# Kernel optimization log

Hardware: AMD Instinct MI355X
Metric: run time of the kernel (lower is better)

The kernel has to match this reference:

```python
import jax, jax.numpy as jnp
import numpy as np
from jax import lax

B, T, D, LSTM, N_MELS, SPK, NOISE = 256, 600, 256, 512, 80, 256, 64
MAX_R = 10
FC1 = 256
FC2 = D // 2  # 128
FILTERS, KSIZE = 32, 31


def _lin(k, out_d, in_d):
    return jax.random.normal(k, (out_d, in_d), jnp.float32) * 0.02


def setup_inputs() -> dict:
    key = jax.random.key(0)
    ks = list(jax.random.split(key, 40))
    nk = iter(ks)
    inp = {
        "encoder_seq": jax.random.normal(next(nk), (B, T, D), jnp.float32),
        "encoder_seq_proj": jax.random.normal(next(nk), (B, T, D), jnp.float32),
        "prenet_in": jax.random.normal(next(nk), (B, N_MELS), jnp.float32),
        "attn_hidden": jax.random.normal(next(nk), (B, D), jnp.float32),
        "rnn1_hidden": jax.random.normal(next(nk), (B, LSTM), jnp.float32),
        "rnn2_hidden": jax.random.normal(next(nk), (B, LSTM), jnp.float32),
        "rnn1_cell": jax.random.normal(next(nk), (B, LSTM), jnp.float32),
        "rnn2_cell": jax.random.normal(next(nk), (B, LSTM), jnp.float32),
        "context_vec": jax.random.normal(next(nk), (B, D), jnp.float32),
        "speaker_embedding": jax.random.normal(next(nk), (B, SPK), jnp.float32),
        "noise_embedding": jax.random.normal(next(nk), (B, NOISE), jnp.float32),
        "attn_cumulative": jax.random.uniform(next(nk), (B, T), jnp.float32),
        "attn_prev": jax.random.uniform(next(nk), (B, T), jnp.float32),
        "phone_len": jax.random.randint(next(nk), (B,), 1, T + 1),
        # PreNet
        "fc1_w": _lin(next(nk), FC1, N_MELS + NOISE), "fc1_b": jnp.zeros((FC1,), jnp.float32),
        "fc2_w": _lin(next(nk), FC2, FC1), "fc2_b": jnp.zeros((FC2,), jnp.float32),
        # LSA
        "conv_w": jax.random.normal(next(nk), (FILTERS, 2, KSIZE), jnp.float32) * 0.1,
        "L_w": _lin(next(nk), D, FILTERS), "L_b": jnp.zeros((D,), jnp.float32),
        "W_w": _lin(next(nk), D, D), "W_b": jnp.zeros((D,), jnp.float32),
        "v_w": _lin(next(nk), 1, D),
        # attn GRU: input = D + D//2 + SPK
        "gru_wih": _lin(next(nk), 3 * D, D + FC2 + SPK), "gru_whh": _lin(next(nk), 3 * D, D),
        "gru_bih": jnp.zeros((3 * D,), jnp.float32), "gru_bhh": jnp.zeros((3 * D,), jnp.float32),
        # rnn_input Linear: 2*D + SPK + NOISE -> LSTM
        "rnn_in_w": _lin(next(nk), LSTM, 2 * D + SPK + NOISE), "rnn_in_b": jnp.zeros((LSTM,), jnp.float32),
        # two LSTMCells
        "l1_wih": _lin(next(nk), 4 * LSTM, LSTM), "l1_whh": _lin(next(nk), 4 * LSTM, LSTM),
        "l1_bih": jnp.zeros((4 * LSTM,), jnp.float32), "l1_bhh": jnp.zeros((4 * LSTM,), jnp.float32),
        "l2_wih": _lin(next(nk), 4 * LSTM, LSTM), "l2_whh": _lin(next(nk), 4 * LSTM, LSTM),
        "l2_bih": jnp.zeros((4 * LSTM,), jnp.float32), "l2_bhh": jnp.zeros((4 * LSTM,), jnp.float32),
        # mel projection (no bias)
        "mel_w": _lin(next(nk), N_MELS * MAX_R, LSTM),
        "r": 2,
    }
    return inp


def _gru(x, h, wih, whh, bih, bhh):
    gi = x @ wih.T + bih
    gh = h @ whh.T + bhh
    i_r, i_z, i_n = jnp.split(gi, 3, axis=-1)
    h_r, h_z, h_n = jnp.split(gh, 3, axis=-1)
    r = jax.nn.sigmoid(i_r + h_r)
    z = jax.nn.sigmoid(i_z + h_z)
    n = jnp.tanh(i_n + r * h_n)
    return (1.0 - z) * n + z * h


def _lstm(x, h, c, wih, whh, bih, bhh):
    g = x @ wih.T + bih + h @ whh.T + bhh
    i, f, gg, o = jnp.split(g, 4, axis=-1)
    c_new = jax.nn.sigmoid(f) * c + jax.nn.sigmoid(i) * jnp.tanh(gg)
    h_new = jax.nn.sigmoid(o) * jnp.tanh(c_new)
    return h_new, c_new


def reference(encoder_seq, encoder_seq_proj, prenet_in, attn_hidden, rnn1_hidden,
              rnn2_hidden, rnn1_cell, rnn2_cell, context_vec, speaker_embedding,
              noise_embedding, attn_cumulative, attn_prev, phone_len,
              fc1_w, fc1_b, fc2_w, fc2_b, conv_w, L_w, L_b, W_w, W_b, v_w,
              gru_wih, gru_whh, gru_bih, gru_bhh, rnn_in_w, rnn_in_b,
              l1_wih, l1_whh, l1_bih, l1_bhh, l2_wih, l2_whh, l2_bih, l2_bhh,
              mel_w, r):
    # PreNet (eval-mode: dropout omitted for a deterministic reference)
    p = jnp.concatenate([prenet_in, noise_embedding], axis=-1)
    p = jax.nn.relu(p @ fc1_w.T + fc1_b)
    prenet_out = jax.nn.relu(p @ fc2_w.T + fc2_b)

    # attention GRU
    attn_rnn_in = jnp.concatenate([context_vec, prenet_out, speaker_embedding], axis=-1)
    attn_hidden = _gru(attn_rnn_in, attn_hidden, gru_wih, gru_whh, gru_bih, gru_bhh)

    # location-sensitive attention (t > 0 step; state passed explicitly)
    pq = (attn_hidden @ W_w.T + W_b)[:, None, :]                     # [B,1,D]
    location = jnp.stack([attn_cumulative, attn_prev], axis=1)       # [B,2,T]
    loc = lax.conv_general_dilated(location, conv_w, (1,), [((KSIZE - 1) // 2,) * 2],
                                   dimension_numbers=("NCH", "OIH", "NCH"))  # [B,F,T]
    pl = jnp.einsum("bft,df->btd", loc, L_w) + L_b                   # [B,T,D]
    u = jnp.einsum("btd,od->bt", jnp.tanh(pq + encoder_seq_proj + pl), v_w)
    mask = jnp.arange(T)[None, :] < phone_len[:, None]
    u = jnp.where(mask, u, -1e9)
    scores_bt = jax.nn.softmax(u, axis=1)                            # [B,T]
    scores = scores_bt[:, None, :]                                   # [B,1,T]

    context_vec = jnp.einsum("bt,btd->bd", scores_bt, encoder_seq)   # [B,D]

    x = jnp.concatenate([context_vec, attn_hidden, speaker_embedding, noise_embedding], axis=1)
    x = x @ rnn_in_w.T + rnn_in_b

    rnn1_hidden, rnn1_cell = _lstm(x, rnn1_hidden, rnn1_cell, l1_wih, l1_whh, l1_bih, l1_bhh)
    x = x + rnn1_hidden
    rnn2_hidden, rnn2_cell = _lstm(x, rnn2_hidden, rnn2_cell, l2_wih, l2_whh, l2_bih, l2_bhh)
    x = x + rnn2_hidden

    mels = (x @ mel_w.T).reshape(B, N_MELS, MAX_R)[:, :, :r]
    return (mels, scores, attn_hidden, rnn1_hidden, rnn2_hidden, rnn1_cell, rnn2_cell, context_vec)
```

## Files before the change

kernel.cpp:

```cpp
#include <hip/hip_runtime.h>
#include <hip/hip_bf16.h>
#include <cstdint>

#define B_ 256
#define T_ 600
#define D_ 256

typedef __attribute__((ext_vector_type(8))) short bf16x8;
typedef __attribute__((ext_vector_type(4))) float f32x4;

__device__ __forceinline__ float fast_sigmoid(float x) {
    return __fdividef(1.0f, 1.0f + __expf(-x));
}
__device__ __forceinline__ float fast_tanh(float x) {
    return 1.0f - __fdividef(2.0f, __expf(2.0f * x) + 1.0f);
}
__device__ __forceinline__ ushort f2bf(float f) {
    unsigned u = __float_as_uint(f);
    u += 0x7FFF + ((u >> 16) & 1);
    return (ushort)(u >> 16);
}

__global__ __launch_bounds__(256) void prenet_kernel(
    const float* __restrict__ pre_in, const float* __restrict__ noise,
    const float* __restrict__ w1, const float* __restrict__ b1,
    const float* __restrict__ w2, const float* __restrict__ b2,
    const float* __restrict__ ctx_in, const float* __restrict__ spk,
    const float* __restrict__ L_w, ushort* __restrict__ Lw16,
    float* __restrict__ Xgru, float* __restrict__ Xrnn)
{
    __shared__ float xin[144];
    __shared__ float p1[256];
    int b = blockIdx.x, t = threadIdx.x;
    if (b == 0) {
        for (int o = t; o < 8192; o += 256) {
            int dt = o >> 9;
            int ln = (o >> 3) & 63;
            int j  = o & 7;
            int in_idx = (dt * 16 + (ln & 15)) * 32 + (ln >> 4) * 8 + j;
            Lw16[o] = f2bf(L_w[in_idx]);
        }
    }
    float s = spk[b * 256 + t];
    Xgru[b * 640 + t] = ctx_in[b * 256 + t];
    Xgru[b * 640 + 384 + t] = s;
    Xrnn[b * 832 + 512 + t] = s;
    if (t < 64) Xrnn[b * 832 + 768 + t] = noise[b * 64 + t];
    if (t < 80) xin[t] = pre_in[b * 80 + t];
    else if (t < 144) xin[t] = noise[b * 64 + (t - 80)];
    __syncthreads();
    float acc = b1[t];
    const float4* w = (const float4*)(w1 + t * 144);
    const float4* xi = (const float4*)xin;
#pragma unroll 9
    for (int k = 0; k < 36; ++k) {
        float4 wv = w[k]; float4 xv = xi[k];
        acc += wv.x * xv.x + wv.y * xv.y + wv.z * xv.z + wv.w * xv.w;
    }
    p1[t] = fmaxf(acc, 0.f);
    __syncthreads();
    if (t < 128) {
        float a2 = b2[t];
        const float4* w2v = (const float4*)(w2 + t * 256);
        const float4* pv = (const float4*)p1;
#pragma unroll 8
        for (int k = 0; k < 64; ++k) {
            float4 wv = w2v[k]; float4 xv = pv[k];
            a2 += wv.x * xv.x + wv.y * xv.y + wv.z * xv.z + wv.w * xv.w;
        }
        Xgru[b * 640 + 256 + t] = fmaxf(a2, 0.f);
    }
}

__global__ __launch_bounds__(256) void convert_w(
    const float* __restrict__ w1ih, const float* __restrict__ w1hh,
    const float* __restrict__ w2ih, const float* __restrict__ w2hh,
    ushort* __restrict__ wcat1, ushort* __restrict__ wcat2)
{
    int n = blockIdx.x & 2047;
    int layer = blockIdx.x >> 11;
    int t = threadIdx.x;
    const float* wih = layer ? w2ih : w1ih;
    const float* whh = layer ? w2hh : w1hh;
    ushort* dst = layer ? wcat2 : wcat1;
    const float* src = (t < 128) ? (wih + (size_t)n * 512 + t * 4)
                                 : (whh + (size_t)n * 512 + (t - 128) * 4);
    float4 v = *(const float4*)src;
    ushort4 o;
    o.x = f2bf(v.x); o.y = f2bf(v.y); o.z = f2bf(v.z); o.w = f2bf(v.w);
    *(ushort4*)&dst[(size_t)n * 1024 + t * 4] = o;
}

__global__ __launch_bounds__(256) void cast_xh(
    const float* __restrict__ x, const float* __restrict__ h,
    ushort* __restrict__ xh)
{
    int b = blockIdx.x, t = threadIdx.x;
    float2 xv = *(const float2*)&x[b * 512 + t * 2];
    float2 hv = *(const float2*)&h[b * 512 + t * 2];
    xh[(size_t)b * 1024 + t * 2 + 0] = f2bf(xv.x);
    xh[(size_t)b * 1024 + t * 2 + 1] = f2bf(xv.y);
    xh[(size_t)b * 1024 + 512 + t * 2 + 0] = f2bf(hv.x);
    xh[(size_t)b * 1024 + 512 + t * 2 + 1] = f2bf(hv.y);
}

__global__ __launch_bounds__(256) void mfma_gemm(
    const ushort* __restrict__ A16, const ushort* __restrict__ B16,
    float* __restrict__ G0, float* __restrict__ G1)
{
    int tid = threadIdx.x;
    int lane = tid & 63, wv = tid >> 6;
    int m0 = blockIdx.x * 32;
    int n0 = blockIdx.y * 64;
    int kbase = blockIdx.z * 512;
    float* Gout = blockIdx.z ? G1 : G0;
    int wm = wv >> 1, wn = wv & 1;
    int cl = lane & 15, ko = (lane >> 4) * 8;

    const ushort* ap  = A16 + (size_t)(m0 + wm * 16 + cl) * 1024 + kbase + ko;
    const ushort* bp0 = B16 + (size_t)(n0 + wn * 32 + cl) * 1024 + kbase + ko;
    const ushort* bp1 = bp0 + (size_t)16 * 1024;

    f32x4 acc0 = {0.f, 0.f, 0.f, 0.f};
    f32x4 acc1 = {0.f, 0.f, 0.f, 0.f};
#pragma unroll
    for (int ks = 0; ks < 16; ++ks) {
        bf16x8 a  = *(const bf16x8*)(ap  + ks * 32);
        bf16x8 b0 = *(const bf16x8*)(bp0 + ks * 32);
        bf16x8 b1 = *(const bf16x8*)(bp1 + ks * 32);
        acc0 = __builtin_amdgcn_mfma_f32_16x16x32_bf16(a, b0, acc0, 0, 0, 0);
        acc1 = __builtin_amdgcn_mfma_f32_16x16x32_bf16(a, b1, acc1, 0, 0, 0);
    }
    int orow = m0 + wm * 16 + (lane >> 4) * 4;
    int ocol = n0 + wn * 32 + cl;
#pragma unroll
    for (int r2 = 0; r2 < 4; ++r2) {
        Gout[(size_t)(orow + r2) * 2048 + ocol]      = acc0[r2];
        Gout[(size_t)(orow + r2) * 2048 + ocol + 16] = acc1[r2];
    }
}

__global__ __launch_bounds__(256) void gemm16(
    const float* __restrict__ A1, int K1, const float* __restrict__ B1,
    const float* __restrict__ A2, int K2, const float* __restrict__ B2,
    const float* __restrict__ bias, float* __restrict__ C, int N)
{
    __shared__ float As[16][17];
    __shared__ float Bs[16][68];
    int tid = threadIdx.x;
    int m0 = blockIdx.x * 16, n0 = blockIdx.y * 64;
    int tm = tid >> 4, tn = tid & 15;
    int lr = tid >> 2, lq = tid & 3;
    int ar = tid >> 2;
    float acc[4] = {};
    int nkt = (K1 + K2) >> 4;

    float4 av, bv;
    {
        const float* A; const float* Bb; int kk; int K;
        if (0 < K1) { A = A1; Bb = B1; kk = 0; K = K1; }
        else        { A = A2; Bb = B2; kk = -K1; K = K2; }
        if (tid < 64) av = *(const float4*)&A[(size_t)(m0 + ar) * K + kk + lq * 4];
        bv = *(const float4*)&Bb[(size_t)(n0 + lr) * K + kk + lq * 4];
    }
    for (int kt = 0; kt < nkt; ++kt) {
        __syncthreads();
        if (tid < 64) {
            As[lq * 4 + 0][ar] = av.x; As[lq * 4 + 1][ar] = av.y;
            As[lq * 4 + 2][ar] = av.z; As[lq * 4 + 3][ar] = av.w;
        }
        Bs[lq * 4 + 0][lr] = bv.x; Bs[lq * 4 + 1][lr] = bv.y;
        Bs[lq * 4 + 2][lr] = bv.z; Bs[lq * 4 + 3][lr] = bv.w;
        __syncthreads();
        if (kt + 1 < nkt) {
            int kg = (kt + 1) << 4;
            const float* A; const float* Bb; int kk; int K;
            if (kg < K1) { A = A1; Bb = B1; kk = kg; K = K1; }
            else         { A = A2; Bb = B2; kk = kg - K1; K = K2; }
            if (tid < 64) av = *(const float4*)&A[(size_t)(m0 + ar) * K + kk + lq * 4];
            bv = *(const float4*)&Bb[(size_t)(n0 + lr) * K + kk + lq * 4];
        }
#pragma unroll
        for (int k = 0; k < 16; ++k) {
            float a = As[k][tm];
            float4 b4 = *(const float4*)&Bs[k][tn * 4];
            acc[0] = fmaf(a, b4.x, acc[0]);
            acc[1] = fmaf(a, b4.y, acc[1]);
            acc[2] = fmaf(a, b4.z, acc[2]);
            acc[3] = fmaf(a, b4.w, acc[3]);
        }
    }
    float4 bb = make_float4(0.f, 0.f, 0.f, 0.f);
    if (bias) bb = *(const float4*)&bias[n0 + tn * 4];
    float4 o = make_float4(acc[0] + bb.x, acc[1] + bb.y, acc[2] + bb.z, acc[3] + bb.w);
    *(float4*)&C[(size_t)(m0 + tm) * N + n0 + tn * 4] = o;
}

__global__ __launch_bounds__(256) void gru_combine(
    const float* __restrict__ Cgi, const float* __restrict__ Cgh,
    const float* __restrict__ h_in, float* __restrict__ ah_out,
    float* __restrict__ Xrnn)
{
    int b = blockIdx.x, j = threadIdx.x;
    float gir = Cgi[b * 768 + j], giz = Cgi[b * 768 + 256 + j], gin = Cgi[b * 768 + 512 + j];
    float ghr = Cgh[b * 768 + j], ghz = Cgh[b * 768 + 256 + j], ghn = Cgh[b * 768 + 512 + j];
    float rr = fast_sigmoid(gir + ghr);
    float zz = fast_sigmoid(giz + ghz);
    float nn = fast_tanh(gin + rr * ghn);
    float h = (1.f - zz) * nn + zz * h_in[b * 256 + j];
    ah_out[b * 256 + j] = h;
    Xrnn[b * 832 + 256 + j] = h;
}

#define TCH 64
__global__ __launch_bounds__(256) void attn_u_kernel(
    const float* __restrict__ esp, const float* __restrict__ pq,
    const float* __restrict__ cum, const float* __restrict__ prv,
    const float* __restrict__ conv_w, const ushort* __restrict__ Lw16,
    const float* __restrict__ L_b, const float* __restrict__ v_w,
    float* __restrict__ u)
{
    __shared__ float cumL[TCH + 32], prvL[TCH + 32];
    __shared__ float cwL[32 * 62];
    __shared__ ushort lwS[8192];
    __shared__ ushort locs[TCH][40];
    __shared__ float pq2s[256], vvs[256];
    int b = blockIdx.y;
    int t0 = blockIdx.x * TCH;
    int tid = threadIdx.x;
    int lane = tid & 63, wv = tid >> 6;
    int cl = lane & 15, gr = lane >> 4;

    for (int i = tid; i < TCH + 30; i += 256) {
        int tg = t0 + i - 15;
        bool ok = (tg >= 0) && (tg < T_);
        cumL[i] = ok ? cum[b * T_ + tg] : 0.f;
        prvL[i] = ok ? prv[b * T_ + tg] : 0.f;
    }
    for (int i = tid; i < 32 * 62; i += 256) cwL[i] = conv_w[i];
    {
        const float4* src = (const float4*)Lw16;
        float4* dst = (float4*)lwS;
#pragma unroll
        for (int i = 0; i < 4; ++i) dst[tid + i * 256] = src[tid + i * 256];
    }
    pq2s[tid] = pq[b * 256 + tid] + L_b[tid];
    vvs[tid] = v_w[tid];

    int tw = t0 + wv * 16 + cl;
    int tc = (tw < T_) ? tw : (T_ - 1);
    const float4* ep4 = (const float4*)(esp + ((size_t)b * T_ + tc) * 256) + gr;
    float e[64];
#pragma unroll
    for (int dt = 0; dt < 16; ++dt) {
        float4 t4 = ep4[dt * 4];
        e[dt * 4 + 0] = t4.x; e[dt * 4 + 1] = t4.y;
        e[dt * 4 + 2] = t4.z; e[dt * 4 + 3] = t4.w;
    }

    asm volatile("s_waitcnt lgkmcnt(0)" ::: "memory");
    __builtin_amdgcn_s_barrier();
    __builtin_amdgcn_sched_barrier(0);

    {
        int f = tid & 31, ts = tid >> 5;
        const float* c0 = &cwL[f * 62];
        float acc[8] = {};
#pragma unroll
        for (int k = 0; k < 31; ++k) {
            float wcv = c0[k], wpv = c0[31 + k];
#pragma unroll
            for (int i = 0; i < 8; ++i)
                acc[i] = fmaf(cumL[ts * 8 + i + k], wcv, fmaf(prvL[ts * 8 + i + k], wpv, acc[i]));
        }
#pragma unroll
        for (int i = 0; i < 8; ++i)
            locs[ts * 8 + i][f] = f2bf(acc[i]);
    }
    __syncthreads();

    bf16x8 locf = *(const bf16x8*)&locs[wv * 16 + cl][gr * 8];
    float sum = 0.f;
#pragma unroll
    for (int dt = 0; dt < 16; ++dt) {
        bf16x8 af = *(const bf16x8*)&lwS[(dt * 64 + lane) * 8];
        float4 pq4 = *(const float4*)&pq2s[dt * 16 + gr * 4];
        float4 vv4 = *(const float4*)&vvs[dt * 16 + gr * 4];
        f32x4 acc = {pq4.x, pq4.y, pq4.z, pq4.w};
        acc = __builtin_amdgcn_mfma_f32_16x16x32_bf16(af, locf, acc, 0, 0, 0);
        sum = fmaf(fast_tanh(e[dt * 4 + 0] + acc[0]), vv4.x, sum);
        sum = fmaf(fast_tanh(e[dt * 4 + 1] + acc[1]), vv4.y, sum);
        sum = fmaf(fast_tanh(e[dt * 4 + 2] + acc[2]), vv4.z, sum);
        sum = fmaf(fast_tanh(e[dt * 4 + 3] + acc[3]), vv4.w, sum);
    }
    sum += __shfl_xor(sum, 16, 64);
    sum += __shfl_xor(sum, 32, 64);
    if (lane < 16 && tw < T_) u[b * T_ + tw] = sum;
}

__global__ __launch_bounds__(1024) void softmax_ctx_kernel(
    const float* __restrict__ u, const int* __restrict__ plen,
    const float* __restrict__ enc,
    float* __restrict__ scores, float* __restrict__ ctx_out,
    float* __restrict__ Xrnn)
{
    __shared__ float sc[T_];
    __shared__ float red[16];
    __shared__ float part[16][256];
    int b = blockIdx.x, tid = threadIdx.x;
    int lane = tid & 63, wid = tid >> 6;
    int pl = plen[b];
    float mv = -1e30f;
    if (tid < T_) {
        float uv = u[b * T_ + tid];
        mv = (tid < pl) ? uv : -1e9f;
        sc[tid] = mv;
    }
    float m = mv;
#pragma unroll
    for (int off = 32; off > 0; off >>= 1) m = fmaxf(m, __shfl_xor(m, off, 64));
    if (lane == 0) red[wid] = m;
    __syncthreads();
    m = red[0];
#pragma unroll
    for (int i = 1; i < 16; ++i) m = fmaxf(m, red[i]);
    float ev = 0.f;
    if (tid < T_) ev = __expf(sc[tid] - m);
    float s = ev;
    __syncthreads();
#pragma unroll
    for (int off = 32; off > 0; off >>= 1) s += __shfl_xor(s, off, 64);
    if (lane == 0) red[wid] = s;
    __syncthreads();
    float tot = 0.f;
#pragma unroll
    for (int i = 0; i < 16; ++i) tot += red[i];
    float inv = __fdividef(1.0f, tot);
    if (tid < T_) {
        float scv = ev * inv;
        scores[b * T_ + tid] = scv;
        sc[tid] = scv;
    }
    __syncthreads();
    float a0 = 0.f, a1 = 0.f, a2 = 0.f, a3 = 0.f;
    const float4* ep = (const float4*)(enc + ((size_t)b * T_ + wid) * 256) + lane;
    for (int t = wid; t < T_; t += 16) {
        float sv = sc[t];
        float4 ev4 = *ep;
        a0 = fmaf(sv, ev4.x, a0);
        a1 = fmaf(sv, ev4.y, a1);
        a2 = fmaf(sv, ev4.z, a2);
        a3 = fmaf(sv, ev4.w, a3);
        ep += 16 * 64;
    }
    part[wid][lane * 4 + 0] = a0;
    part[wid][lane * 4 + 1] = a1;
    part[wid][lane * 4 + 2] = a2;
    part[wid][lane * 4 + 3] = a3;
    __syncthreads();
    if (tid < 256) {
        float c = 0.f;
#pragma unroll
        for (int q = 0; q < 16; ++q) c += part[q][tid];
        ctx_out[b * 256 + tid] = c;
        Xrnn[b * 832 + tid] = c;
    }
}

__global__ __launch_bounds__(512) void lstm_combine2(
    const float* __restrict__ G0, const float* __restrict__ G1,
    const float* __restrict__ bih, const float* __restrict__ bhh,
    const float* __restrict__ c_in, const float* __restrict__ x_in,
    float* __restrict__ h_out, float* __restrict__ c_out,
    float* __restrict__ x_next,
    const float* __restrict__ h_next_in, ushort* __restrict__ xh_next)
{
    int b = blockIdx.x, j = threadIdx.x;
    size_t base = (size_t)b * 2048;
    float gi = G0[base + j] + G1[base + j] + bih[j] + bhh[j];
    float gf = G0[base + 512 + j] + G1[base + 512 + j] + bih[512 + j] + bhh[512 + j];
    float gg = G0[base + 1024 + j] + G1[base + 1024 + j] + bih[1024 + j] + bhh[1024 + j];
    float go = G0[base + 1536 + j] + G1[base + 1536 + j] + bih[1536 + j] + bhh[1536 + j];
    float c = fast_sigmoid(gf) * c_in[b * 512 + j] + fast_sigmoid(gi) * fast_tanh(gg);
    float h = fast_sigmoid(go) * fast_tanh(c);
    float xn = x_in[b * 512 + j] + h;
    h_out[b * 512 + j] = h;
    c_out[b * 512 + j] = c;
    x_next[b * 512 + j] = xn;
    if (xh_next) {
        xh_next[(size_t)b * 1024 + j] = f2bf(xn);
        xh_next[(size_t)b * 1024 + 512 + j] = f2bf(h_next_in[b * 512 + j]);
    }
}

__global__ __launch_bounds__(256) void mel_kernel(
    const float* __restrict__ x2, const float* __restrict__ mel_w,
    int r, float* __restrict__ mels)
{
    __shared__ float xl[512];
    int b = blockIdx.x, tid = threadIdx.x;
    xl[tid] = x2[b * 512 + tid];
    xl[256 + tid] = x2[b * 512 + 256 + tid];
    __syncthreads();
    for (int idx = tid; idx < 80 * r; idx += 256) {
        int mrow = (idx / r) * 10 + (idx % r);
        const float4* w = (const float4*)(mel_w + (size_t)mrow * 512);
        const float4* xv = (const float4*)xl;
        float acc = 0.f;
#pragma unroll 16
        for (int k = 0; k < 128; ++k) {
            float4 a = w[k], c = xv[k];
            acc += a.x * c.x + a.y * c.y + a.z * c.z + a.w * c.w;
        }
        mels[(size_t)b * 80 * r + idx] = acc;
    }
}

extern "C" void kernel_launch(void* const* d_in, const int* in_sizes, int n_in,
                              void* d_out, int out_size, void* d_ws, size_t ws_size,
                              hipStream_t stream)
{
    const float* enc    = (const float*)d_in[0];
    const float* esp    = (const float*)d_in[1];
    const float* pre_in = (const float*)d_in[2];
    const float* ah_in  = (const float*)d_in[3];
    const float* h1_in  = (const float*)d_in[4];
    const float* h2_in  = (const float*)d_in[5];
    const float* c1_in  = (const float*)d_in[6];
    const float* c2_in  = (const float*)d_in[7];
    const float* ctx_in = (const float*)d_in[8];
    const float* spk    = (const float*)d_in[9];
    const float* noise  = (const float*)d_in[10];
    const float* cum    = (const float*)d_in[11];
    const float* prv    = (const float*)d_in[12];
    const int*   plen   = (const int*)d_in[13];
    const float* fc1_w  = (const float*)d_in[14];
    const float* fc1_b  = (const float*)d_in[15];
    const float* fc2_w  = (const float*)d_in[16];
    const float* fc2_b  = (const float*)d_in[17];
    const float* conv_w = (const float*)d_in[18];
    const float* L_w    = (const float*)d_in[19];
    const float* L_b    = (const float*)d_in[20];
    const float* W_w    = (const float*)d_in[21];
    const float* W_b    = (const float*)d_in[22];
    const float* v_w    = (const float*)d_in[23];
    const float* g_wih  = (const float*)d_in[24];
    const float* g_whh  = (const float*)d_in[25];
    const float* g_bih  = (const float*)d_in[26];
    const float* g_bhh  = (const float*)d_in[27];
    const float* ri_w   = (const float*)d_in[28];
    const float* ri_b   = (const float*)d_in[29];
    const float* l1_wih = (const float*)d_in[30];
    const float* l1_whh = (const float*)d_in[31];
    const float* l1_bih = (const float*)d_in[32];
    const float* l1_bhh = (const float*)d_in[33];
    const float* l2_wih = (const float*)d_in[34];
    const float* l2_whh = (const float*)d_in[35];
    const float* l2_bih = (const float*)d_in[36];
    const float* l2_bhh = (const float*)d_in[37];
    const float* mel_w  = (const float*)d_in[38];

    int r = (out_size - 808960) / 20480;
    if (r < 1) r = 1;
    if (r > 10) r = 10;

    float* out    = (float*)d_out;
    float* mels   = out;
    float* scores = out + (size_t)20480 * r;
    float* ah_out = scores + 153600;
    float* h1_out = ah_out + 65536;
    float* h2_out = h1_out + 131072;
    float* c1_out = h2_out + 131072;
    float* c2_out = c1_out + 131072;
    float* ctx_out = c2_out + 131072;

    float* ws   = (float*)d_ws;
    float* Xgru = ws;
    float* Cgi  = Xgru + 163840;
    float* Cgh  = Cgi + 196608;
    float* pq   = Cgh + 196608;
    float* uu   = pq + 65536;
    float* Xrnn = uu + 153600;
    float* x0   = Xrnn + 212992;
    float* x1   = x0 + 131072;
    float* x2   = x1 + 131072;
    float* G0   = x2 + 131072;
    float* G1   = G0 + 524288;
    ushort* Lw16  = (ushort*)(G1 + 524288);
    ushort* wcat1 = Lw16 + 8192;
    ushort* wcat2 = wcat1 + 2097152;
    ushort* xh1   = wcat2 + 2097152;
    ushort* xh2   = xh1 + 262144;

    prenet_kernel<<<256, 256, 0, stream>>>(pre_in, noise, fc1_w, fc1_b, fc2_w, fc2_b,
                                           ctx_in, spk, L_w, Lw16, Xgru, Xrnn);
    convert_w<<<4096, 256, 0, stream>>>(l1_wih, l1_whh, l2_wih, l2_whh, wcat1, wcat2);
    gemm16<<<dim3(16, 12), 256, 0, stream>>>(Xgru, 640, g_wih, nullptr, 0, nullptr, g_bih, Cgi, 768);
    gemm16<<<dim3(16, 12), 256, 0, stream>>>(ah_in, 256, g_whh, nullptr, 0, nullptr, g_bhh, Cgh, 768);
    gru_combine<<<256, 256, 0, stream>>>(Cgi, Cgh, ah_in, ah_out, Xrnn);
    gemm16<<<dim3(16, 4), 256, 0, stream>>>(ah_out, 256, W_w, nullptr, 0, nullptr, W_b, pq, 256);
    attn_u_kernel<<<dim3(10, 256), 256, 0, stream>>>(esp, pq, cum, prv, conv_w, Lw16, L_b, v_w, uu);
    softmax_ctx_kernel<<<256, 1024, 0, stream>>>(uu, plen, enc, scores, ctx_out, Xrnn);
    gemm16<<<dim3(16, 8), 256, 0, stream>>>(Xrnn, 832, ri_w, nullptr, 0, nullptr, ri_b, x0, 512);
    cast_xh<<<256, 256, 0, stream>>>(x0, h1_in, xh1);
    mfma_gemm<<<dim3(8, 32, 2), 256, 0, stream>>>(xh1, wcat1, G0, G1);
    lstm_combine2<<<256, 512, 0, stream>>>(G0, G1, l1_bih, l1_bhh, c1_in, x0,
                                           h1_out, c1_out, x1, h2_in, xh2);
    mfma_gemm<<<dim3(8, 32, 2), 256, 0, stream>>>(xh2, wcat2, G0, G1);
    lstm_combine2<<<256, 512, 0, stream>>>(G0, G1, l2_bih, l2_bhh, c2_in, x1,
                                           h2_out, c2_out, x2, nullptr, nullptr);
    mel_kernel<<<256, 256, 0, stream>>>(x2, mel_w, r, mels);
}
```

Measured before the change: 217.0 us.

## Replace fp32 SIMT gemm16 with bf16 MFMA GEMMs and fuse weight casts

All four remaining fp32 shared-memory GEMMs (GRU input/hidden, W query projection, rnn_input) now run through a generic bf16 MFMA kernel. Activations are written as bf16 directly by their producer kernels. All weight and input casts are merged into one conversion launch, and the rnn_input GEMM epilogue also writes the bf16 xh1 buffer, which removes the cast_xh launch. This trades extra per-call weight conversion traffic and reduced precision for matrix-core throughput and fewer launches.

```diff
diff --git a/kernel.cpp b/kernel.cpp
--- a/kernel.cpp
+++ b/kernel.cpp
@@ -27,7 +27,7 @@
     const float* __restrict__ w2, const float* __restrict__ b2,
     const float* __restrict__ ctx_in, const float* __restrict__ spk,
     const float* __restrict__ L_w, ushort* __restrict__ Lw16,
-    float* __restrict__ Xgru, float* __restrict__ Xrnn)
+    ushort* __restrict__ Xgru16, ushort* __restrict__ Xrnn16)
 {
     __shared__ float xin[144];
     __shared__ float p1[256];
@@ -42,10 +42,10 @@
         }
     }
     float s = spk[b * 256 + t];
-    Xgru[b * 640 + t] = ctx_in[b * 256 + t];
-    Xgru[b * 640 + 384 + t] = s;
-    Xrnn[b * 832 + 512 + t] = s;
-    if (t < 64) Xrnn[b * 832 + 768 + t] = noise[b * 64 + t];
+    Xgru16[b * 640 + t] = f2bf(ctx_in[b * 256 + t]);
+    Xgru16[b * 640 + 384 + t] = f2bf(s);
+    Xrnn16[b * 832 + 512 + t] = f2bf(s);
+    if (t < 64) Xrnn16[b * 832 + 768 + t] = f2bf(noise[b * 64 + t]);
     if (t < 80) xin[t] = pre_in[b * 80 + t];
     else if (t < 144) xin[t] = noise[b * 64 + (t - 80)];
     __syncthreads();
@@ -68,40 +68,103 @@
             float4 wv = w2v[k]; float4 xv = pv[k];
             a2 += wv.x * xv.x + wv.y * xv.y + wv.z * xv.z + wv.w * xv.w;
         }
-        Xgru[b * 640 + 256 + t] = fmaxf(a2, 0.f);
-    }
-}
-
-__global__ __launch_bounds__(256) void convert_w(
+        Xgru16[b * 640 + 256 + t] = f2bf(fmaxf(a2, 0.f));
+    }
+}
+
+__global__ __launch_bounds__(256) void convert_all(
     const float* __restrict__ w1ih, const float* __restrict__ w1hh,
     const float* __restrict__ w2ih, const float* __restrict__ w2hh,
-    ushort* __restrict__ wcat1, ushort* __restrict__ wcat2)
-{
-    int n = blockIdx.x & 2047;
-    int layer = blockIdx.x >> 11;
-    int t = threadIdx.x;
-    const float* wih = layer ? w2ih : w1ih;
-    const float* whh = layer ? w2hh : w1hh;
-    ushort* dst = layer ? wcat2 : wcat1;
-    const float* src = (t < 128) ? (wih + (size_t)n * 512 + t * 4)
-                                 : (whh + (size_t)n * 512 + (t - 128) * 4);
-    float4 v = *(const float4*)src;
+    const float* __restrict__ gwih, const float* __restrict__ gwhh,
+    const float* __restrict__ Ww, const float* __restrict__ riw,
+    const float* __restrict__ ahin, const float* __restrict__ h1in,
+    ushort* __restrict__ wcat1, ushort* __restrict__ wcat2,
+    ushort* __restrict__ gwih16, ushort* __restrict__ gwhh16,
+    ushort* __restrict__ Ww16, ushort* __restrict__ riw16,
+    ushort* __restrict__ ahin16, ushort* __restrict__ xh1)
+{
+    int bid = blockIdx.x, t = threadIdx.x;
+    if (bid < 4096) {
+        int n = bid & 2047;
+        int layer = bid >> 11;
+        const float* wih = layer ? w2ih : w1ih;
+        const float* whh = layer ? w2hh : w1hh;
+        ushort* dst = layer ? wcat2 : wcat1;
+        const float* src = (t < 128) ? (wih + (size_t)n * 512 + t * 4)
+                                     : (whh + (size_t)n * 512 + (t - 128) * 4);
+        float4 v = *(const float4*)src;
+        ushort4 o;
+        o.x = f2bf(v.x); o.y = f2bf(v.y); o.z = f2bf(v.z); o.w = f2bf(v.w);
+        *(ushort4*)&dst[(size_t)n * 1024 + t * 4] = o;
+        return;
+    }
+    bid -= 4096;
+    if (bid >= 1216) {
+        bid -= 1216;
+        size_t i = (size_t)bid * 1024 + t * 4;
+        float4 v = *(const float4*)&h1in[i];
+        int b = (int)(i >> 9), k = (int)(i & 511);
+        ushort4 o;
+        o.x = f2bf(v.x); o.y = f2bf(v.y); o.z = f2bf(v.z); o.w = f2bf(v.w);
+        *(ushort4*)&xh1[(size_t)b * 1024 + 512 + k] = o;
+        return;
+    }
+    const float* src; ushort* dst;
+    if (bid < 480)       { src = gwih; dst = gwih16; }
+    else if (bid < 672)  { bid -= 480;  src = gwhh; dst = gwhh16; }
+    else if (bid < 736)  { bid -= 672;  src = Ww;   dst = Ww16; }
+    else if (bid < 1152) { bid -= 736;  src = riw;  dst = riw16; }
+    else                 { bid -= 1152; src = ahin; dst = ahin16; }
+    size_t i = (size_t)bid * 1024 + t * 4;
+    float4 v = *(const float4*)&src[i];
     ushort4 o;
     o.x = f2bf(v.x); o.y = f2bf(v.y); o.z = f2bf(v.z); o.w = f2bf(v.w);
-    *(ushort4*)&dst[(size_t)n * 1024 + t * 4] = o;
-}
-
-__global__ __launch_bounds__(256) void cast_xh(
-    const float* __restrict__ x, const float* __restrict__ h,
-    ushort* __restrict__ xh)
-{
-    int b = blockIdx.x, t = threadIdx.x;
-    float2 xv = *(const float2*)&x[b * 512 + t * 2];
-    float2 hv = *(const float2*)&h[b * 512 + t * 2];
-    xh[(size_t)b * 1024 + t * 2 + 0] = f2bf(xv.x);
-    xh[(size_t)b * 1024 + t * 2 + 1] = f2bf(xv.y);
-    xh[(size_t)b * 1024 + 512 + t * 2 + 0] = f2bf(hv.x);
-    xh[(size_t)b * 1024 + 512 + t * 2 + 1] = f2bf(hv.y);
+    *(ushort4*)&dst[i] = o;
+}
+
+__global__ __launch_bounds__(256) void mfma_gemmN(
+    const ushort* __restrict__ A16, int K,
+    const ushort* __restrict__ B16, const float* __restrict__ bias,
+    float* __restrict__ C, int N, ushort* __restrict__ xcast)
+{
+    int tid = threadIdx.x;
+    int lane = tid & 63, wv = tid >> 6;
+    int m0 = blockIdx.x * 32;
+    int n0 = blockIdx.y * 64;
+    int wm = wv >> 1, wn = wv & 1;
+    int cl = lane & 15, ko = (lane >> 4) * 8;
+
+    const ushort* ap  = A16 + (size_t)(m0 + wm * 16 + cl) * K + ko;
+    const ushort* bp0 = B16 + (size_t)(n0 + wn * 32 + cl) * K + ko;
+    const ushort* bp1 = bp0 + (size_t)16 * K;
+
+    f32x4 acc0 = {0.f, 0.f, 0.f, 0.f};
+    f32x4 acc1 = {0.f, 0.f, 0.f, 0.f};
+    int nks = K >> 5;
+#pragma unroll 2
+    for (int ks = 0; ks < nks; ++ks) {
+        bf16x8 a  = *(const bf16x8*)ap;
+        bf16x8 b0 = *(const bf16x8*)bp0;
+        bf16x8 b1 = *(const bf16x8*)bp1;
+        ap += 32; bp0 += 32; bp1 += 32;
+        acc0 = __builtin_amdgcn_mfma_f32_16x16x32_bf16(a, b0, acc0, 0, 0, 0);
+        acc1 = __builtin_amdgcn_mfma_f32_16x16x32_bf16(a, b1, acc1, 0, 0, 0);
+    }
+    int orow = m0 + wm * 16 + (lane >> 4) * 4;
+    int ocol = n0 + wn * 32 + cl;
+    float bb0 = bias ? bias[ocol] : 0.f;
+    float bb1 = bias ? bias[ocol + 16] : 0.f;
+#pragma unroll
+    for (int r2 = 0; r2 < 4; ++r2) {
+        float v0 = acc0[r2] + bb0;
+        float v1 = acc1[r2] + bb1;
+        C[(size_t)(orow + r2) * N + ocol]      = v0;
+        C[(size_t)(orow + r2) * N + ocol + 16] = v1;
+        if (xcast) {
+            xcast[(size_t)(orow + r2) * 1024 + ocol]      = f2bf(v0);
+            xcast[(size_t)(orow + r2) * 1024 + ocol + 16] = f2bf(v1);
+        }
+    }
 }
 
 __global__ __launch_bounds__(256) void mfma_gemm(
@@ -140,66 +203,10 @@
     }
 }
 
-__global__ __launch_bounds__(256) void gemm16(
-    const float* __restrict__ A1, int K1, const float* __restrict__ B1,
-    const float* __restrict__ A2, int K2, const float* __restrict__ B2,
-    const float* __restrict__ bias, float* __restrict__ C, int N)
-{
-    __shared__ float As[16][17];
-    __shared__ float Bs[16][68];
-    int tid = threadIdx.x;
-    int m0 = blockIdx.x * 16, n0 = blockIdx.y * 64;
-    int tm = tid >> 4, tn = tid & 15;
-    int lr = tid >> 2, lq = tid & 3;
-    int ar = tid >> 2;
-    float acc[4] = {};
-    int nkt = (K1 + K2) >> 4;
-
-    float4 av, bv;
-    {
-        const float* A; const float* Bb; int kk; int K;
-        if (0 < K1) { A = A1; Bb = B1; kk = 0; K = K1; }
-        else        { A = A2; Bb = B2; kk = -K1; K = K2; }
-        if (tid < 64) av = *(const float4*)&A[(size_t)(m0 + ar) * K + kk + lq * 4];
-        bv = *(const float4*)&Bb[(size_t)(n0 + lr) * K + kk + lq * 4];
-    }
-    for (int kt = 0; kt < nkt; ++kt) {
-        __syncthreads();
-        if (tid < 64) {
-            As[lq * 4 + 0][ar] = av.x; As[lq * 4 + 1][ar] = av.y;
-            As[lq * 4 + 2][ar] = av.z; As[lq * 4 + 3][ar] = av.w;
-        }
-        Bs[lq * 4 + 0][lr] = bv.x; Bs[lq * 4 + 1][lr] = bv.y;
-        Bs[lq * 4 + 2][lr] = bv.z; Bs[lq * 4 + 3][lr] = bv.w;
-        __syncthreads();
-        if (kt + 1 < nkt) {
-            int kg = (kt + 1) << 4;
-            const float* A; const float* Bb; int kk; int K;
-            if (kg < K1) { A = A1; Bb = B1; kk = kg; K = K1; }
-            else         { A = A2; Bb = B2; kk = kg - K1; K = K2; }
-            if (tid < 64) av = *(const float4*)&A[(size_t)(m0 + ar) * K + kk + lq * 4];
-            bv = *(const float4*)&Bb[(size_t)(n0 + lr) * K + kk + lq * 4];
-        }
-#pragma unroll
-        for (int k = 0; k < 16; ++k) {
-            float a = As[k][tm];
-            float4 b4 = *(const float4*)&Bs[k][tn * 4];
-            acc[0] = fmaf(a, b4.x, acc[0]);
-            acc[1] = fmaf(a, b4.y, acc[1]);
-            acc[2] = fmaf(a, b4.z, acc[2]);
-            acc[3] = fmaf(a, b4.w, acc[3]);
-        }
-    }
-    float4 bb = make_float4(0.f, 0.f, 0.f, 0.f);
-    if (bias) bb = *(const float4*)&bias[n0 + tn * 4];
-    float4 o = make_float4(acc[0] + bb.x, acc[1] + bb.y, acc[2] + bb.z, acc[3] + bb.w);
-    *(float4*)&C[(size_t)(m0 + tm) * N + n0 + tn * 4] = o;
-}
-
 __global__ __launch_bounds__(256) void gru_combine(
     const float* __restrict__ Cgi, const float* __restrict__ Cgh,
     const float* __restrict__ h_in, float* __restrict__ ah_out,
-    float* __restrict__ Xrnn)
+    ushort* __restrict__ ah16, ushort* __restrict__ Xrnn16)
 {
     int b = blockIdx.x, j = threadIdx.x;
     float gir = Cgi[b * 768 + j], giz = Cgi[b * 768 + 256 + j], gin = Cgi[b * 768 + 512 + j];
@@ -209,7 +216,8 @@
     float nn = fast_tanh(gin + rr * ghn);
     float h = (1.f - zz) * nn + zz * h_in[b * 256 + j];
     ah_out[b * 256 + j] = h;
-    Xrnn[b * 832 + 256 + j] = h;
+    ah16[b * 256 + j] = f2bf(h);
+    Xrnn16[b * 832 + 256 + j] = f2bf(h);
 }
 
 #define TCH 64
@@ -302,7 +310,7 @@
     const float* __restrict__ u, const int* __restrict__ plen,
     const float* __restrict__ enc,
     float* __restrict__ scores, float* __restrict__ ctx_out,
-    float* __restrict__ Xrnn)
+    ushort* __restrict__ Xrnn16)
 {
     __shared__ float sc[T_];
     __shared__ float red[16];
@@ -363,7 +371,7 @@
 #pragma unroll
         for (int q = 0; q < 16; ++q) c += part[q][tid];
         ctx_out[b * 256 + tid] = c;
-        Xrnn[b * 832 + tid] = c;
+        Xrnn16[b * 832 + tid] = f2bf(c);
     }
 }
 
@@ -475,34 +483,42 @@
     float* ctx_out = c2_out + 131072;
 
     float* ws   = (float*)d_ws;
-    float* Xgru = ws;
-    float* Cgi  = Xgru + 163840;
+    float* Cgi  = ws;
     float* Cgh  = Cgi + 196608;
     float* pq   = Cgh + 196608;
     float* uu   = pq + 65536;
-    float* Xrnn = uu + 153600;
-    float* x0   = Xrnn + 212992;
+    float* x0   = uu + 153600;
     float* x1   = x0 + 131072;
     float* x2   = x1 + 131072;
     float* G0   = x2 + 131072;
     float* G1   = G0 + 524288;
-    ushort* Lw16  = (ushort*)(G1 + 524288);
-    ushort* wcat1 = Lw16 + 8192;
-    ushort* wcat2 = wcat1 + 2097152;
-    ushort* xh1   = wcat2 + 2097152;
-    ushort* xh2   = xh1 + 262144;
+    ushort* Lw16   = (ushort*)(G1 + 524288);
+    ushort* Xgru16 = Lw16 + 8192;
+    ushort* Xrnn16 = Xgru16 + 163840;
+    ushort* ah16   = Xrnn16 + 212992;
+    ushort* ahin16 = ah16 + 65536;
+    ushort* wcat1  = ahin16 + 65536;
+    ushort* wcat2  = wcat1 + 2097152;
+    ushort* gwih16 = wcat2 + 2097152;
+    ushort* gwhh16 = gwih16 + 491520;
+    ushort* Ww16   = gwhh16 + 196608;
+    ushort* riw16  = Ww16 + 65536;
+    ushort* xh1    = riw16 + 425984;
+    ushort* xh2    = xh1 + 262144;
 
     prenet_kernel<<<256, 256, 0, stream>>>(pre_in, noise, fc1_w, fc1_b, fc2_w, fc2_b,
-                                           ctx_in, spk, L_w, Lw16, Xgru, Xrnn);
-    convert_w<<<4096, 256, 0, stream>>>(l1_wih, l1_whh, l2_wih, l2_whh, wcat1, wcat2);
-    gemm16<<<dim3(16, 12), 256, 0, stream>>>(Xgru, 640, g_wih, nullptr, 0, nullptr, g_bih, Cgi, 768);
-    gemm16<<<dim3(16, 12), 256, 0, stream>>>(ah_in, 256, g_whh, nullptr, 0, nullptr, g_bhh, Cgh, 768);
-    gru_combine<<<256, 256, 0, stream>>>(Cgi, Cgh, ah_in, ah_out, Xrnn);
-    gemm16<<<dim3(16, 4), 256, 0, stream>>>(ah_out, 256, W_w, nullptr, 0, nullptr, W_b, pq, 256);
+                                           ctx_in, spk, L_w, Lw16, Xgru16, Xrnn16);
+    convert_all<<<5440, 256, 0, stream>>>(l1_wih, l1_whh, l2_wih, l2_whh,
+                                          g_wih, g_whh, W_w, ri_w, ah_in, h1_in,
+                                          wcat1, wcat2, gwih16, gwhh16,
+                                          Ww16, riw16, ahin16, xh1);
+    mfma_gemmN<<<dim3(8, 12), 256, 0, stream>>>(Xgru16, 640, gwih16, g_bih, Cgi, 768, nullptr);
+    mfma_gemmN<<<dim3(8, 12), 256, 0, stream>>>(ahin16, 256, gwhh16, g_bhh, Cgh, 768, nullptr);
+    gru_combine<<<256, 256, 0, stream>>>(Cgi, Cgh, ah_in, ah_out, ah16, Xrnn16);
+    mfma_gemmN<<<dim3(8, 4), 256, 0, stream>>>(ah16, 256, Ww16, W_b, pq, 256, nullptr);
     attn_u_kernel<<<dim3(10, 256), 256, 0, stream>>>(esp, pq, cum, prv, conv_w, Lw16, L_b, v_w, uu);
-    softmax_ctx_kernel<<<256, 1024, 0, stream>>>(uu, plen, enc, scores, ctx_out, Xrnn);
-    gemm16<<<dim3(16, 8), 256, 0, stream>>>(Xrnn, 832, ri_w, nullptr, 0, nullptr, ri_b, x0, 512);
-    cast_xh<<<256, 256, 0, stream>>>(x0, h1_in, xh1);
+    softmax_ctx_kernel<<<256, 1024, 0, stream>>>(uu, plen, enc, scores, ctx_out, Xrnn16);
+    mfma_gemmN<<<dim3(8, 8), 256, 0, stream>>>(Xrnn16, 832, riw16, ri_b, x0, 512, xh1);
     mfma_gemm<<<dim3(8, 32, 2), 256, 0, stream>>>(xh1, wcat1, G0, G1);
     lstm_combine2<<<256, 512, 0, stream>>>(G0, G1, l1_bih, l1_bhh, c1_in, x0,
                                            h1_out, c1_out, x1, h2_in, xh2);
```

Result: faster. 188.4 us (median of 2 runs) (-13.2%).
